# Kernel optimization log

Hardware: AMD Instinct MI355X
Metric: run time of the kernel (lower is better)

Reference implementation:

```python
import jax, jax.numpy as jnp
import numpy as np

N, IN_DIM = 50000, 1024
E = 100000
NUM_REL = 40
HEADS, OUT_DIM = 4, 200
HID = HEADS * OUT_DIM  # 800
B = 8192
NEG_SLOPE = 0.2


def setup_inputs() -> dict:
    key = jax.random.key(0)
    ks = jax.random.split(key, 12)
    node_emb = jax.random.normal(ks[0], (N, IN_DIM), dtype=jnp.float32)
    # RelGAT learnable params
    W = jax.random.normal(ks[1], (IN_DIM, HID), dtype=jnp.float32) * (1.0 / np.sqrt(IN_DIM))
    bias = jnp.zeros((HID,), dtype=jnp.float32)
    a_src = jax.random.normal(ks[2], (HEADS, OUT_DIM), dtype=jnp.float32) * 0.1
    a_dst = jax.random.normal(ks[3], (HEADS, OUT_DIM), dtype=jnp.float32) * 0.1
    a_rel = jax.random.normal(ks[4], (HEADS, OUT_DIM), dtype=jnp.float32) * 0.1
    rel_feat = jax.random.normal(ks[5], (NUM_REL, HID), dtype=jnp.float32) * 0.1
    # DistMult scorer relation embeddings
    rel_emb = jax.random.normal(ks[6], (NUM_REL, HID), dtype=jnp.float32) * 0.1
    # Graph structure (constants)
    edge_index = jax.random.randint(ks[7], (2, E), 0, N, dtype=jnp.int64)
    edge_type = jax.random.randint(ks[8], (E,), 0, NUM_REL, dtype=jnp.int64)
    # Triple batch
    src_ids = jax.random.randint(ks[9], (B,), 0, N, dtype=jnp.int64)
    rel_ids = jax.random.randint(ks[10], (B,), 0, NUM_REL, dtype=jnp.int64)
    dst_ids = jax.random.randint(ks[11], (B,), 0, N, dtype=jnp.int64)
    return dict(node_emb=node_emb, W=W, bias=bias, a_src=a_src, a_dst=a_dst,
                a_rel=a_rel, rel_feat=rel_feat, rel_emb=rel_emb,
                edge_index=edge_index, edge_type=edge_type,
                src_ids=src_ids, rel_ids=rel_ids, dst_ids=dst_ids)


def _rel_gat(node_emb, W, bias, a_src, a_dst, a_rel, rel_feat, edge_index, edge_type):
    src, dst = edge_index[0], edge_index[1]
    h = (node_emb @ W).reshape(N, HEADS, OUT_DIM)          # [N,H,D]
    hs = h[src]                                            # [E,H,D] gather
    hd = h[dst]                                            # [E,H,D] gather
    r = rel_feat[edge_type].reshape(E, HEADS, OUT_DIM)     # [E,H,D]
    # relation-conditioned attention logits per head
    logits = (jnp.einsum('ehd,hd->eh', hs, a_src)
              + jnp.einsum('ehd,hd->eh', hd, a_dst)
              + jnp.einsum('ehd,hd->eh', r, a_rel))        # [E,H]
    logits = jax.nn.leaky_relu(logits, NEG_SLOPE)
    # segment softmax over incoming edges of each destination node
    seg_max = jax.ops.segment_max(logits, dst, num_segments=N)   # [N,H]
    e = jnp.exp(logits - seg_max[dst])                           # [E,H]
    denom = jax.ops.segment_sum(e, dst, num_segments=N)          # [N,H]
    alpha = e / denom[dst]                                       # [E,H]
    # weighted scatter-aggregate of source messages
    out = jax.ops.segment_sum(alpha[:, :, None] * hs, dst, num_segments=N)  # [N,H,D]
    return out.reshape(N, HID) + bias                            # dropout: eval mode (identity)


def reference(node_emb, W, bias, a_src, a_dst, a_rel, rel_feat, rel_emb,
              edge_index, edge_type, src_ids, rel_ids, dst_ids):
    refined = _rel_gat(node_emb, W, bias, a_src, a_dst, a_rel, rel_feat,
                       edge_index, edge_type)                # [N, HID]
    src_vec = refined[src_ids]                               # [B, HID]
    dst_vec = refined[dst_ids]                               # [B, HID]
    # DistMult: sum(s * r * d)
    scores = jnp.sum(src_vec * rel_emb[rel_ids] * dst_vec, axis=-1)  # [B]
    return scores
```

## Files before the change

kernel.cpp:

```cpp
#include <hip/hip_runtime.h>
#include <hip/hip_bf16.h>
#include <math.h>

#define NN 50000
#define IN_DIM 1024
#define EE 100000
#define NUM_REL 40
#define HEADS 4
#define OUT_D 200
#define HID 800
#define BB 8192
#define SLOT_CAP 16384
#define SRC_CAP 50176

typedef __attribute__((ext_vector_type(8))) short short8;
typedef __attribute__((ext_vector_type(4))) float f32x4;

__device__ inline unsigned short f2bf(float f) {
    unsigned int u = __float_as_uint(f);
    u += 0x7FFF + ((u >> 16) & 1);
    return (unsigned short)(u >> 16);
}
__device__ inline float bf2f(unsigned short s) {
    return __uint_as_float(((unsigned int)s) << 16);
}
__device__ inline void gl2lds16(const unsigned short* g, unsigned short* l) {
    __builtin_amdgcn_global_load_lds(
        (const __attribute__((address_space(1))) void*)g,
        (__attribute__((address_space(3))) void*)l, 16, 0, 0);
}

__global__ void k_init(int* slot_of_node, int* xrow_of_node, int* deg, int* counters) {
    int i = blockIdx.x * 256 + threadIdx.x;
    if (i < NN) { slot_of_node[i] = -1; xrow_of_node[i] = -1; }
    if (i < SLOT_CAP) deg[i] = 0;
    if (i < 8) counters[i] = 0;
}

__global__ void k_build_slots(const int* src_ids, const int* dst_ids,
                              int* slot_of_node, int* counters, int* scorelist) {
    int i = blockIdx.x * 256 + threadIdx.x;
    if (i >= 2 * BB) return;
    int n = (i < BB) ? src_ids[i] : dst_ids[i - BB];
    if (slot_of_node[n] == -1) {
        if (atomicCAS(&slot_of_node[n], -1, -2) == -1) {
            int s = atomicAdd(&counters[0], 1);
            slot_of_node[n] = s;
            scorelist[s] = n;
        }
    }
}

__global__ void k_wa(const float* W, const float* a_src, const float* a_dst,
                     const float* a_rel, const float* rel_feat,
                     float* Wa, float* prel) {
    int tid = blockIdx.x * 256 + threadIdx.x;
    if (tid < IN_DIM * 8) {
        int k = tid >> 3, c = tid & 7;
        const float* a = (c < 4) ? a_src : a_dst;
        int h = c & 3;
        float s = 0.f;
        for (int d = 0; d < OUT_D; ++d)
            s += W[k * HID + h * OUT_D + d] * a[h * OUT_D + d];
        Wa[k * 8 + c] = s;
    } else if (tid < IN_DIM * 8 + NUM_REL * HEADS) {
        int j = tid - IN_DIM * 8;
        int r = j >> 2, h = j & 3;
        float s = 0.f;
        for (int d = 0; d < OUT_D; ++d)
            s += rel_feat[r * HID + h * OUT_D + d] * a_rel[h * OUT_D + d];
        prel[j] = s;
    }
}

__global__ void k_edge0(const int* ei, const int* slot_of_node,
                        int* xrow_of_node, int* counters, int* rows, int* deg) {
    int e = blockIdx.x * 256 + threadIdx.x;
    if (e >= EE) return;
    int dn = ei[EE + e];
    int slot = slot_of_node[dn];
    if (slot < 0) return;
    int sn = ei[e];
    if (xrow_of_node[sn] == -1) {
        if (atomicCAS(&xrow_of_node[sn], -1, -2) == -1) {
            int t = atomicAdd(&counters[1], 1);
            rows[t] = sn;
            xrow_of_node[sn] = t;
        }
    }
    atomicAdd(&deg[slot], 1);
}

__global__ void k_tail(const int* scorelist, int* xrow_of_node, int* counters, int* rows) {
    int i = blockIdx.x * 256 + threadIdx.x;
    if (i >= counters[0]) return;
    int n = scorelist[i];
    if (xrow_of_node[n] < 0) {
        int t = atomicAdd(&counters[3], 1);
        int xr = counters[1] + t;
        xrow_of_node[n] = xr;
        rows[xr] = n;
    }
}

__global__ __launch_bounds__(256) void k_scan(const int* deg, int* base, int* cursor) {
    __shared__ int pref[257];
    int t = threadIdx.x;
    int s = 0;
    for (int i = 0; i < SLOT_CAP / 256; ++i) s += deg[t * (SLOT_CAP / 256) + i];
    pref[t + 1] = s;
    if (t == 0) pref[0] = 0;
    __syncthreads();
    if (t == 0)
        for (int i = 1; i <= 256; ++i) pref[i] += pref[i - 1];
    __syncthreads();
    int r = pref[t];
    for (int i = 0; i < SLOT_CAP / 256; ++i) {
        int idx = t * (SLOT_CAP / 256) + i;
        base[idx] = r;
        cursor[idx] = r;
        r += deg[idx];
    }
}

__global__ __launch_bounds__(256) void k_gather_cast(const float* x, const int* rows,
                                                     const int* counters, unsigned short* xg) {
    int nneed = counters[1] + counters[3];
    int gid = blockIdx.x * 256 + threadIdx.x;
    int row = gid >> 7;
    if (row >= nneed) return;
    int j = (gid & 127) * 8;
    int node = rows[row];
    const float* src = x + (size_t)node * IN_DIM + j;
    float4 a = *(const float4*)(src);
    float4 b = *(const float4*)(src + 4);
    unsigned short o[8] = {f2bf(a.x), f2bf(a.y), f2bf(a.z), f2bf(a.w),
                           f2bf(b.x), f2bf(b.y), f2bf(b.z), f2bf(b.w)};
    *(short8*)(xg + (size_t)row * IN_DIM + j) = *(short8*)o;
}

__global__ __launch_bounds__(256) void k_wt(const float* W, const float* Wa,
                                            unsigned short* Wt) {
    __shared__ float tile[64][65];
    int k0 = blockIdx.x * 64, c0 = blockIdx.y * 64;
    int t = threadIdx.x;
    {
        int kk = t >> 2, cc = (t & 3) * 16;
        for (int i = 0; i < 16; ++i) {
            int c = c0 + cc + i;
            float v = 0.f;
            if (c < HID) v = W[(size_t)(k0 + kk) * HID + c];
            else if (c < HID + 8) v = Wa[(size_t)(k0 + kk) * 8 + (c - HID)];
            tile[cc + i][kk] = v;
        }
    }
    __syncthreads();
    {
        int cc = t >> 2, kk = (t & 3) * 16;
        unsigned short o[16];
        for (int i = 0; i < 16; ++i) o[i] = f2bf(tile[cc][kk + i]);
        *(short8*)(Wt + (size_t)(c0 + cc) * IN_DIM + k0 + kk) = *(short8*)o;
        *(short8*)(Wt + (size_t)(c0 + cc) * IN_DIM + k0 + kk + 8) = *(short8*)(o + 8);
    }
}

#define GBM 128
#define GBN 128
#define GBK 32
__global__ __launch_bounds__(256) void k_hgemm(const unsigned short* xg, const unsigned short* Wt,
                                               const int* counters, unsigned short* h_src,
                                               float* sS, float* sD) {
    int nsrc = counters[1];
    int nneed = nsrc + counters[3];
    int col0 = blockIdx.x * GBN;
    int row0 = blockIdx.y * GBM;
    int rowlim = (col0 == 768) ? nneed : nsrc;
    if (row0 >= rowlim) return;
    __shared__ unsigned short As[GBM * GBK];
    __shared__ unsigned short Bs[GBN * GBK];
    int t = threadIdx.x;
    int sg = t >> 6, sfq = (t >> 4) & 3, sfm = t & 15;
    const unsigned short* a0 = xg + (size_t)(row0 + sg * 16 + sfm) * IN_DIM + sfq * 8;
    const unsigned short* a1 = a0 + (size_t)64 * IN_DIM;
    const unsigned short* b0 = Wt + (size_t)(col0 + sg * 16 + sfm) * IN_DIM + sfq * 8;
    const unsigned short* b1 = b0 + (size_t)64 * IN_DIM;
    unsigned short* la0 = As + t * 8;
    unsigned short* la1 = As + (256 + t) * 8;
    unsigned short* lb0 = Bs + t * 8;
    unsigned short* lb1 = Bs + (256 + t) * 8;
    int w = t >> 6, lane = t & 63;
    int ga = (w >> 1) * 4, gb = (w & 1) * 4;
    int wr = (w >> 1) * 64, wc = (w & 1) * 64;
    int fm = lane & 15, fq = lane >> 4;
    f32x4 acc[4][4] = {};
    for (int k0 = 0; k0 < IN_DIM; k0 += GBK) {
        __syncthreads();
        gl2lds16(a0 + k0, la0);
        gl2lds16(a1 + k0, la1);
        gl2lds16(b0 + k0, lb0);
        gl2lds16(b1 + k0, lb1);
        __syncthreads();
        short8 af[4], bf[4];
#pragma unroll
        for (int i = 0; i < 4; ++i)
            af[i] = *(const short8*)&As[((ga + i) * 64 + lane) * 8];
#pragma unroll
        for (int j = 0; j < 4; ++j)
            bf[j] = *(const short8*)&Bs[((gb + j) * 64 + lane) * 8];
#pragma unroll
        for (int i = 0; i < 4; ++i)
#pragma unroll
            for (int j = 0; j < 4; ++j)
                acc[i][j] = __builtin_amdgcn_mfma_f32_16x16x32_bf16(af[i], bf[j], acc[i][j], 0, 0, 0);
    }
#pragma unroll
    for (int i = 0; i < 4; ++i) {
#pragma unroll
        for (int j = 0; j < 4; ++j) {
            int gcol = col0 + wc + j * 16 + fm;
            if (gcol >= HID + 8) continue;
#pragma unroll
            for (int r = 0; r < 4; ++r) {
                int grow = row0 + wr + i * 16 + fq * 4 + r;
                float v = acc[i][j][r];
                if (gcol < HID) {
                    if (grow < nsrc) h_src[(size_t)grow * HID + gcol] = f2bf(v);
                } else if (grow < nneed) {
                    int c = gcol - HID;
                    if (c < 4) sS[grow * 4 + c] = v;
                    else sD[grow * 4 + (c - 4)] = v;
                }
            }
        }
    }
}

__global__ void k_place(const int* ei, const int* etype, const int* slot_of_node,
                        const int* xrow_of_node, int* cursor,
                        const float* sS, const float* sD, const float* prel,
                        float* clogit, int* tlist) {
    int e = blockIdx.x * 256 + threadIdx.x;
    if (e >= EE) return;
    int dn = ei[EE + e];
    int slot = slot_of_node[dn];
    if (slot < 0) return;
    int sn = ei[e];
    int r = etype[e];
    int xs = xrow_of_node[sn];
    int xd = xrow_of_node[dn];
    int pos = atomicAdd(&cursor[slot], 1);
    tlist[pos] = xs;
    float4 lg;
    float* lp = (float*)&lg;
#pragma unroll
    for (int h = 0; h < 4; ++h) {
        float v = sS[xs * 4 + h] + sD[xd * 4 + h] + prel[r * 4 + h];
        lp[h] = v > 0.f ? v : 0.2f * v;
    }
    *(float4*)&clogit[(size_t)pos * 4] = lg;
}

__global__ __launch_bounds__(256) void k_aggregate(const int* counters, const int* base,
                                                   const int* deg, const int* tlist,
                                                   const float* clogit,
                                                   const unsigned short* h_src, const float* bias,
                                                   float* refined) {
    int b = blockIdx.x;
    if (b >= counters[0]) return;
    int beg = base[b], d = deg[b];
    __shared__ float m4[4], den4[4];
    __shared__ float alpha[64][4];
    __shared__ int tsl[64];
    int t = threadIdx.x;
    if (t < 4) {
        float m = -3e38f;
        for (int j = 0; j < d; ++j)
            m = fmaxf(m, clogit[(size_t)(beg + j) * 4 + t]);
        float s = 0.f;
        for (int j = 0; j < d; ++j)
            s += expf(clogit[(size_t)(beg + j) * 4 + t] - m);
        m4[t] = m;
        den4[t] = s;
    }
    __syncthreads();
    int h0 = t / 200, h1 = (t + 256) / 200, h2 = (t + 512) / 200;
    float acc0 = 0.f, acc1 = 0.f, acc2 = 0.f, acc3 = 0.f;
    for (int j0 = 0; j0 < d; j0 += 64) {
        int nc = min(64, d - j0);
        if (t < nc * 4) {
            int j = t >> 2, h = t & 3;
            alpha[j][h] = expf(clogit[(size_t)(beg + j0 + j) * 4 + h] - m4[h]) / den4[h];
            if (h == 0) tsl[j] = tlist[beg + j0 + j];
        }
        __syncthreads();
        for (int j = 0; j < nc; ++j) {
            const unsigned short* hr = h_src + (size_t)tsl[j] * HID;
            acc0 += alpha[j][h0] * bf2f(hr[t]);
            acc1 += alpha[j][h1] * bf2f(hr[t + 256]);
            acc2 += alpha[j][h2] * bf2f(hr[t + 512]);
            if (t < 32) acc3 += alpha[j][3] * bf2f(hr[768 + t]);
        }
        __syncthreads();
    }
    float* rr = refined + (size_t)b * HID;
    rr[t] = acc0 + bias[t];
    rr[t + 256] = acc1 + bias[t + 256];
    rr[t + 512] = acc2 + bias[t + 512];
    if (t < 32) rr[768 + t] = acc3 + bias[768 + t];
}

__global__ __launch_bounds__(256) void k_score(const int* src_ids, const int* rel_ids,
                                               const int* dst_ids, const int* slot_of_node,
                                               const float* rel_emb, const float* refined,
                                               float* out) {
    int gid = blockIdx.x * 256 + threadIdx.x;
    int b = gid >> 6;
    int lane = threadIdx.x & 63;
    if (b >= BB) return;
    int ss = slot_of_node[src_ids[b]];
    int ds = slot_of_node[dst_ids[b]];
    int r = rel_ids[b];
    const float* sv = refined + (size_t)ss * HID;
    const float* dv = refined + (size_t)ds * HID;
    const float* rv = rel_emb + (size_t)r * HID;
    float acc = 0.f;
    for (int c4 = lane; c4 < 200; c4 += 64) {
        float4 s = *(const float4*)(sv + c4 * 4);
        float4 dq = *(const float4*)(dv + c4 * 4);
        float4 rr = *(const float4*)(rv + c4 * 4);
        acc += s.x * rr.x * dq.x + s.y * rr.y * dq.y + s.z * rr.z * dq.z + s.w * rr.w * dq.w;
    }
    for (int off = 32; off; off >>= 1) acc += __shfl_down(acc, off, 64);
    if (lane == 0) out[b] = acc;
}

extern "C" void kernel_launch(void* const* d_in, const int* in_sizes, int n_in,
                              void* d_out, int out_size, void* d_ws, size_t ws_size,
                              hipStream_t stream) {
    const float* node_emb = (const float*)d_in[0];
    const float* W        = (const float*)d_in[1];
    const float* bias     = (const float*)d_in[2];
    const float* a_src    = (const float*)d_in[3];
    const float* a_dst    = (const float*)d_in[4];
    const float* a_rel    = (const float*)d_in[5];
    const float* rel_feat = (const float*)d_in[6];
    const float* rel_emb  = (const float*)d_in[7];
    const int* edge_index = (const int*)d_in[8];
    const int* edge_type  = (const int*)d_in[9];
    const int* src_ids    = (const int*)d_in[10];
    const int* rel_ids    = (const int*)d_in[11];
    const int* dst_ids    = (const int*)d_in[12];
    float* out = (float*)d_out;

    char* w = (char*)d_ws;
    auto alloc = [&](size_t bytes) -> void* {
        void* p = (void*)w;
        w += (bytes + 255) & ~(size_t)255;
        return p;
    };
    int* slot_of_node = (int*)alloc((size_t)NN * 4);
    int* xrow_of_node = (int*)alloc((size_t)NN * 4);
    int* scorelist    = (int*)alloc((size_t)SLOT_CAP * 4);
    int* rows         = (int*)alloc((size_t)NN * 4);
    int* counters     = (int*)alloc(256);
    int* deg          = (int*)alloc((size_t)SLOT_CAP * 4);
    int* base         = (int*)alloc((size_t)SLOT_CAP * 4);
    int* cursor       = (int*)alloc((size_t)SLOT_CAP * 4);
    int* tlist        = (int*)alloc((size_t)EE * 4);
    float* clogit = (float*)alloc((size_t)EE * 4 * 4);
    float* sS     = (float*)alloc((size_t)SRC_CAP * 4 * 4);
    float* sD     = (float*)alloc((size_t)SRC_CAP * 4 * 4);
    float* Wa     = (float*)alloc((size_t)IN_DIM * 8 * 4);
    float* prel   = (float*)alloc((size_t)NUM_REL * 4 * 4);
    unsigned short* xg    = (unsigned short*)alloc((size_t)SRC_CAP * IN_DIM * 2);
    unsigned short* Wt    = (unsigned short*)alloc((size_t)896 * IN_DIM * 2);
    unsigned short* h_src = (unsigned short*)alloc((size_t)SRC_CAP * HID * 2);
    float* refined = (float*)alloc((size_t)SLOT_CAP * HID * 4);

    k_init<<<256, 256, 0, stream>>>(slot_of_node, xrow_of_node, deg, counters);
    k_build_slots<<<(2 * BB + 255) / 256, 256, 0, stream>>>(src_ids, dst_ids, slot_of_node,
                                                            counters, scorelist);
    k_wa<<<(IN_DIM * 8 + NUM_REL * HEADS + 255) / 256, 256, 0, stream>>>(
        W, a_src, a_dst, a_rel, rel_feat, Wa, prel);
    k_edge0<<<(EE + 255) / 256, 256, 0, stream>>>(edge_index, slot_of_node,
                                                  xrow_of_node, counters, rows, deg);
    k_tail<<<(SLOT_CAP + 255) / 256, 256, 0, stream>>>(scorelist, xrow_of_node, counters, rows);
    k_scan<<<1, 256, 0, stream>>>(deg, base, cursor);
    k_gather_cast<<<(NN * 128 + 255) / 256, 256, 0, stream>>>(node_emb, rows, counters, xg);
    k_wt<<<dim3(IN_DIM / 64, 896 / 64), 256, 0, stream>>>(W, Wa, Wt);
    dim3 ggrid(896 / GBN, (SRC_CAP + GBM - 1) / GBM);
    k_hgemm<<<ggrid, 256, 0, stream>>>(xg, Wt, counters, h_src, sS, sD);
    k_place<<<(EE + 255) / 256, 256, 0, stream>>>(edge_index, edge_type, slot_of_node,
                                                  xrow_of_node, cursor, sS, sD, prel,
                                                  clogit, tlist);
    k_aggregate<<<SLOT_CAP, 256, 0, stream>>>(counters, base, deg, tlist,
                                              clogit, h_src, bias, refined);
    k_score<<<(BB * 64 + 255) / 256, 256, 0, stream>>>(src_ids, rel_ids, dst_ids,
                                                       slot_of_node, rel_emb, refined, out);
}
```

Measured before the change: 548.8 us.

## Widen GEMM column tile to 256, warp-reduce Wa dots, vectorize scan

```diff
diff --git a/kernel.cpp b/kernel.cpp
--- a/kernel.cpp
+++ b/kernel.cpp
@@ -12,6 +12,7 @@
 #define BB 8192
 #define SLOT_CAP 16384
 #define SRC_CAP 50176
+#define WT_COLS 1024
 
 typedef __attribute__((ext_vector_type(8))) short short8;
 typedef __attribute__((ext_vector_type(4))) float f32x4;
@@ -51,25 +52,36 @@
     }
 }
 
-__global__ void k_wa(const float* W, const float* a_src, const float* a_dst,
-                     const float* a_rel, const float* rel_feat,
-                     float* Wa, float* prel) {
-    int tid = blockIdx.x * 256 + threadIdx.x;
-    if (tid < IN_DIM * 8) {
-        int k = tid >> 3, c = tid & 7;
-        const float* a = (c < 4) ? a_src : a_dst;
-        int h = c & 3;
-        float s = 0.f;
-        for (int d = 0; d < OUT_D; ++d)
-            s += W[k * HID + h * OUT_D + d] * a[h * OUT_D + d];
-        Wa[k * 8 + c] = s;
-    } else if (tid < IN_DIM * 8 + NUM_REL * HEADS) {
-        int j = tid - IN_DIM * 8;
-        int r = j >> 2, h = j & 3;
-        float s = 0.f;
-        for (int d = 0; d < OUT_D; ++d)
-            s += rel_feat[r * HID + h * OUT_D + d] * a_rel[h * OUT_D + d];
-        prel[j] = s;
+__global__ __launch_bounds__(256) void k_wa(const float* W, const float* a_src,
+                                            const float* a_dst, const float* a_rel,
+                                            const float* rel_feat, float* Wa, float* prel) {
+    int wid = blockIdx.x * 4 + (threadIdx.x >> 6);
+    int lane = threadIdx.x & 63;
+    if (wid >= IN_DIM * 8 + NUM_REL * HEADS) return;
+    float acc = 0.f;
+    int d = lane * 4;
+    if (d < OUT_D) {
+        const float* row;
+        const float* a;
+        if (wid < IN_DIM * 8) {
+            int k = wid >> 3, c = wid & 7;
+            int h = c & 3;
+            row = W + (size_t)k * HID + h * OUT_D;
+            a = ((c < 4) ? a_src : a_dst) + h * OUT_D;
+        } else {
+            int j = wid - IN_DIM * 8;
+            int r = j >> 2, h = j & 3;
+            row = rel_feat + (size_t)r * HID + h * OUT_D;
+            a = a_rel + h * OUT_D;
+        }
+        float4 wv = *(const float4*)(row + d);
+        float4 av = *(const float4*)(a + d);
+        acc = wv.x * av.x + wv.y * av.y + wv.z * av.z + wv.w * av.w;
+    }
+    for (int off = 32; off; off >>= 1) acc += __shfl_down(acc, off, 64);
+    if (lane == 0) {
+        if (wid < IN_DIM * 8) Wa[wid] = acc;
+        else prel[wid - IN_DIM * 8] = acc;
     }
 }
 
@@ -107,7 +119,11 @@
     __shared__ int pref[257];
     int t = threadIdx.x;
     int s = 0;
-    for (int i = 0; i < SLOT_CAP / 256; ++i) s += deg[t * (SLOT_CAP / 256) + i];
+    const int4* dv = (const int4*)(deg + t * (SLOT_CAP / 256));
+    for (int i = 0; i < SLOT_CAP / 256 / 4; ++i) {
+        int4 v = dv[i];
+        s += v.x + v.y + v.z + v.w;
+    }
     pref[t + 1] = s;
     if (t == 0) pref[0] = 0;
     __syncthreads();
@@ -165,7 +181,7 @@
 }
 
 #define GBM 128
-#define GBN 128
+#define GBN 256
 #define GBK 32
 __global__ __launch_bounds__(256) void k_hgemm(const unsigned short* xg, const unsigned short* Wt,
                                                const int* counters, unsigned short* h_src,
@@ -179,44 +195,50 @@
     __shared__ unsigned short As[GBM * GBK];
     __shared__ unsigned short Bs[GBN * GBK];
     int t = threadIdx.x;
-    int sg = t >> 6, sfq = (t >> 4) & 3, sfm = t & 15;
-    const unsigned short* a0 = xg + (size_t)(row0 + sg * 16 + sfm) * IN_DIM + sfq * 8;
+    int crow = ((t >> 6) << 4) + (t & 15), coff = ((t >> 4) & 3) << 3;
+    const unsigned short* a0 = xg + (size_t)(row0 + crow) * IN_DIM + coff;
     const unsigned short* a1 = a0 + (size_t)64 * IN_DIM;
-    const unsigned short* b0 = Wt + (size_t)(col0 + sg * 16 + sfm) * IN_DIM + sfq * 8;
+    const unsigned short* b0 = Wt + (size_t)(col0 + crow) * IN_DIM + coff;
     const unsigned short* b1 = b0 + (size_t)64 * IN_DIM;
+    const unsigned short* b2 = b0 + (size_t)128 * IN_DIM;
+    const unsigned short* b3 = b0 + (size_t)192 * IN_DIM;
     unsigned short* la0 = As + t * 8;
     unsigned short* la1 = As + (256 + t) * 8;
     unsigned short* lb0 = Bs + t * 8;
     unsigned short* lb1 = Bs + (256 + t) * 8;
+    unsigned short* lb2 = Bs + (512 + t) * 8;
+    unsigned short* lb3 = Bs + (768 + t) * 8;
     int w = t >> 6, lane = t & 63;
-    int ga = (w >> 1) * 4, gb = (w & 1) * 4;
-    int wr = (w >> 1) * 64, wc = (w & 1) * 64;
+    int ga = (w >> 1) * 4, gb = (w & 1) * 8;
+    int wr = (w >> 1) * 64, wc = (w & 1) * 128;
     int fm = lane & 15, fq = lane >> 4;
-    f32x4 acc[4][4] = {};
+    f32x4 acc[4][8] = {};
     for (int k0 = 0; k0 < IN_DIM; k0 += GBK) {
         __syncthreads();
         gl2lds16(a0 + k0, la0);
         gl2lds16(a1 + k0, la1);
         gl2lds16(b0 + k0, lb0);
         gl2lds16(b1 + k0, lb1);
+        gl2lds16(b2 + k0, lb2);
+        gl2lds16(b3 + k0, lb3);
         __syncthreads();
-        short8 af[4], bf[4];
+        short8 af[4], bf[8];
 #pragma unroll
         for (int i = 0; i < 4; ++i)
             af[i] = *(const short8*)&As[((ga + i) * 64 + lane) * 8];
 #pragma unroll
-        for (int j = 0; j < 4; ++j)
+        for (int j = 0; j < 8; ++j)
             bf[j] = *(const short8*)&Bs[((gb + j) * 64 + lane) * 8];
 #pragma unroll
         for (int i = 0; i < 4; ++i)
 #pragma unroll
-            for (int j = 0; j < 4; ++j)
+            for (int j = 0; j < 8; ++j)
                 acc[i][j] = __builtin_amdgcn_mfma_f32_16x16x32_bf16(af[i], bf[j], acc[i][j], 0, 0, 0);
     }
 #pragma unroll
     for (int i = 0; i < 4; ++i) {
 #pragma unroll
-        for (int j = 0; j < 4; ++j) {
+        for (int j = 0; j < 8; ++j) {
             int gcol = col0 + wc + j * 16 + fm;
             if (gcol >= HID + 8) continue;
 #pragma unroll
@@ -373,22 +395,22 @@
     float* Wa     = (float*)alloc((size_t)IN_DIM * 8 * 4);
     float* prel   = (float*)alloc((size_t)NUM_REL * 4 * 4);
     unsigned short* xg    = (unsigned short*)alloc((size_t)SRC_CAP * IN_DIM * 2);
-    unsigned short* Wt    = (unsigned short*)alloc((size_t)896 * IN_DIM * 2);
+    unsigned short* Wt    = (unsigned short*)alloc((size_t)WT_COLS * IN_DIM * 2);
     unsigned short* h_src = (unsigned short*)alloc((size_t)SRC_CAP * HID * 2);
     float* refined = (float*)alloc((size_t)SLOT_CAP * HID * 4);
 
     k_init<<<256, 256, 0, stream>>>(slot_of_node, xrow_of_node, deg, counters);
     k_build_slots<<<(2 * BB + 255) / 256, 256, 0, stream>>>(src_ids, dst_ids, slot_of_node,
                                                             counters, scorelist);
-    k_wa<<<(IN_DIM * 8 + NUM_REL * HEADS + 255) / 256, 256, 0, stream>>>(
+    k_wa<<<(IN_DIM * 8 + NUM_REL * HEADS + 3) / 4, 256, 0, stream>>>(
         W, a_src, a_dst, a_rel, rel_feat, Wa, prel);
     k_edge0<<<(EE + 255) / 256, 256, 0, stream>>>(edge_index, slot_of_node,
                                                   xrow_of_node, counters, rows, deg);
     k_tail<<<(SLOT_CAP + 255) / 256, 256, 0, stream>>>(scorelist, xrow_of_node, counters, rows);
     k_scan<<<1, 256, 0, stream>>>(deg, base, cursor);
     k_gather_cast<<<(NN * 128 + 255) / 256, 256, 0, stream>>>(node_emb, rows, counters, xg);
-    k_wt<<<dim3(IN_DIM / 64, 896 / 64), 256, 0, stream>>>(W, Wa, Wt);
-    dim3 ggrid(896 / GBN, (SRC_CAP + GBM - 1) / GBM);
+    k_wt<<<dim3(IN_DIM / 64, WT_COLS / 64), 256, 0, stream>>>(W, Wa, Wt);
+    dim3 ggrid(WT_COLS / GBN, (SRC_CAP + GBM - 1) / GBM);
     k_hgemm<<<ggrid, 256, 0, stream>>>(xg, Wt, counters, h_src, sS, sD);
     k_place<<<(EE + 255) / 256, 256, 0, stream>>>(edge_index, edge_type, slot_of_node,
                                                   xrow_of_node, cursor, sS, sD, prel,
```

Result: slower. 614.5 us (+12.0%).
